# Optimization experiments

Hardware: AMD Instinct MI355X
Metric: run time of the kernel (lower is better)

The kernel has to match this reference:

```python
import jax, jax.numpy as jnp
import numpy as np

BATCH = 4
N1 = 131072   # stage-1 voxels (total over batch)
N2 = 32768    # stage-2 (stride-2 downsampled) voxels
D_MODEL = 128
D_INNER = 2 * D_MODEL
D_STATE = 16
D_CONV = 4
DT_RANK = 8   # ceil(d_model / 16)
EPS = 1e-5


def _ln(x, g, b):
    mu = x.mean(-1, keepdims=True)
    v = ((x - mu) ** 2).mean(-1, keepdims=True)
    return (x - mu) * jax.lax.rsqrt(v + EPS) * g + b


def _causal_conv(x, w, b):
    # x: [B,L,Di], w: [Di,K] -> depthwise causal conv1d
    y = jax.lax.conv_general_dilated(
        x.transpose(0, 2, 1), w[:, None, :], (1,), [(D_CONV - 1, 0)],
        dimension_numbers=('NCH', 'OIH', 'NCH'), feature_group_count=D_INNER)
    return y.transpose(0, 2, 1) + b


def _mamba_block(x, ln_g, ln_b, in_w, conv_w, conv_b, xproj_w, dtproj_w, dtproj_b, A_log, Dp, out_w):
    # create_block: LayerNorm -> Mamba mixer (selective scan); returns hidden states
    h = _ln(x, ln_g, ln_b)
    xz = h @ in_w.T                          # [B,L,2*Di]
    xc, z = jnp.split(xz, 2, axis=-1)
    xc = jax.nn.silu(_causal_conv(xc, conv_w, conv_b))
    dbl = xc @ xproj_w.T                     # [B,L,dt_rank+2*d_state]
    dt = jax.nn.softplus(dbl[..., :DT_RANK] @ dtproj_w.T + dtproj_b)  # [B,L,Di]
    Bm = dbl[..., DT_RANK:DT_RANK + D_STATE]
    Cm = dbl[..., DT_RANK + D_STATE:]
    A = -jnp.exp(A_log)                      # [Di,ds]

    def step(hst, inp):
        dt_t, b_t, c_t, u_t = inp            # [B,Di],[B,ds],[B,ds],[B,Di]
        hst = jnp.exp(dt_t[..., None] * A) * hst + (dt_t * u_t)[..., None] * b_t[:, None, :]
        return hst, jnp.einsum('bds,bs->bd', hst, c_t)

    h0 = jnp.zeros((x.shape[0], D_INNER, D_STATE), x.dtype)
    xs = (dt.transpose(1, 0, 2), Bm.transpose(1, 0, 2), Cm.transpose(1, 0, 2), xc.transpose(1, 0, 2))
    _, ys = jax.lax.scan(step, h0, xs)       # ys: [L,B,Di]
    y = ys.transpose(1, 0, 2) + xc * Dp
    y = y * jax.nn.silu(z)
    return y @ out_w.T


def _mamba_params(key):
    ks = jax.random.split(key, 6)
    s = lambda k, sh, sc: jax.random.normal(k, sh, jnp.float32) * sc
    return dict(
        ln_g=jnp.ones((D_MODEL,), jnp.float32), ln_b=jnp.zeros((D_MODEL,), jnp.float32),
        in_w=s(ks[0], (2 * D_INNER, D_MODEL), 0.05),
        conv_w=s(ks[1], (D_INNER, D_CONV), 0.2), conv_b=jnp.zeros((D_INNER,), jnp.float32),
        xproj_w=s(ks[2], (DT_RANK + 2 * D_STATE, D_INNER), 0.05),
        dtproj_w=s(ks[3], (D_INNER, DT_RANK), 0.1), dtproj_b=s(ks[4], (D_INNER,), 0.1),
        A_log=jnp.log(jnp.tile(jnp.arange(1, D_STATE + 1, dtype=jnp.float32), (D_INNER, 1))),
        D=jnp.ones((D_INNER,), jnp.float32),
        out_w=s(ks[5], (D_MODEL, D_INNER), 0.05))


def setup_inputs():
    key = jax.random.key(0)
    k = jax.random.split(key, 10)
    inp = {
        'feats_s1': jax.random.normal(k[0], (N1, D_MODEL), jnp.float32),
        'feats_s2': jax.random.normal(k[1], (N2, D_MODEL), jnp.float32),
        'pos_s1': jax.random.uniform(k[2], (N1, 3), jnp.float32),
        'pos_s2': jax.random.uniform(k[3], (N2, 3), jnp.float32),
        'hilbert_s1': jax.random.randint(k[4], (N1,), 0, 1 << 30, jnp.int32),
        'hilbert_s2': jax.random.randint(k[5], (N2,), 0, 1 << 30, jnp.int32),
        'pe_w': jax.random.normal(k[6], (D_MODEL, 3), jnp.float32) * 0.1,
        'pe_b': jnp.zeros((D_MODEL,), jnp.float32),
        'norm_g': jnp.ones((D_MODEL,), jnp.float32), 'norm_b': jnp.zeros((D_MODEL,), jnp.float32),
        'normb_g': jnp.ones((D_MODEL,), jnp.float32), 'normb_b': jnp.zeros((D_MODEL,), jnp.float32),
    }
    for pref, kk in (('m1_', k[7]), ('m2_', k[8])):
        for n, v in _mamba_params(kk).items():
            inp[pref + n] = v
    return inp


def _forward(feats_s1, feats_s2, pos_s1, pos_s2, pe_w, pe_b, norm_g, norm_b, normb_g, normb_b,
             m1_ln_g, m1_ln_b, m1_in_w, m1_conv_w, m1_conv_b, m1_xproj_w, m1_dtproj_w, m1_dtproj_b, m1_A_log, m1_D, m1_out_w,
             m2_ln_g, m2_ln_b, m2_in_w, m2_conv_w, m2_conv_b, m2_xproj_w, m2_dtproj_w, m2_dtproj_b, m2_A_log, m2_D, m2_out_w,
             hilbert_s1, hilbert_s2):
    L1, L2 = N1 // BATCH, N2 // BATCH
    m1 = (m1_ln_g, m1_ln_b, m1_in_w, m1_conv_w, m1_conv_b, m1_xproj_w, m1_dtproj_w, m1_dtproj_b, m1_A_log, m1_D, m1_out_w)
    m2 = (m2_ln_g, m2_ln_b, m2_in_w, m2_conv_w, m2_conv_b, m2_xproj_w, m2_dtproj_w, m2_dtproj_b, m2_A_log, m2_D, m2_out_w)

    # stage 2: hilbert-order forward scan through mamba_layer1
    f2 = (feats_s2 + pos_s2 @ pe_w.T + pe_b).reshape(BATCH, L2, D_MODEL)
    o2 = jnp.argsort(hilbert_s2.reshape(BATCH, L2), axis=-1)          # inds_curt_to_next
    seq2 = jnp.take_along_axis(f2, o2[..., None], axis=1)
    out2 = _mamba_block(seq2, *m1)
    back2 = jnp.take_along_axis(out2, jnp.argsort(o2, axis=-1)[..., None], axis=1).reshape(N2, D_MODEL)
    out_s2 = _ln(back2, norm_g, norm_b)

    # stage 1: flipped hilbert-order (backward) scan through mamba_layer2
    f1 = (feats_s1 + pos_s1 @ pe_w.T + pe_b).reshape(BATCH, L1, D_MODEL)
    o1 = jnp.argsort(hilbert_s1.reshape(BATCH, L1), axis=-1)
    seq1 = jnp.take_along_axis(f1, o1[..., None], axis=1)[:, ::-1, :]
    out1 = _mamba_block(seq1, *m2)[:, ::-1, :]
    back1 = jnp.take_along_axis(out1, jnp.argsort(o1, axis=-1)[..., None], axis=1).reshape(N1, D_MODEL)
    out_s1 = _ln(back1, normb_g, normb_b)

    return jnp.concatenate([out_s1, out_s2], axis=0)   # [N1+N2, d_model]


def reference(feats_s1, feats_s2, pos_s1, pos_s2, pe_w, pe_b, norm_g, norm_b, normb_g, normb_b,
              m1_ln_g, m1_ln_b, m1_in_w, m1_conv_w, m1_conv_b, m1_xproj_w, m1_dtproj_w, m1_dtproj_b, m1_A_log, m1_D, m1_out_w,
              m2_ln_g, m2_ln_b, m2_in_w, m2_conv_w, m2_conv_b, m2_xproj_w, m2_dtproj_w, m2_dtproj_b, m2_A_log, m2_D, m2_out_w,
              hilbert_s1, hilbert_s2):
    return _forward(feats_s1, feats_s2, pos_s1, pos_s2, pe_w, pe_b, norm_g, norm_b, normb_g, normb_b,
                    m1_ln_g, m1_ln_b, m1_in_w, m1_conv_w, m1_conv_b, m1_xproj_w, m1_dtproj_w, m1_dtproj_b, m1_A_log, m1_D, m1_out_w,
                    m2_ln_g, m2_ln_b, m2_in_w, m2_conv_w, m2_conv_b, m2_xproj_w, m2_dtproj_w, m2_dtproj_b, m2_A_log, m2_D, m2_out_w,
                    hilbert_s1, hilbert_s2)
```

## Files before the change

kernel.cpp:

```cpp
#include <hip/hip_runtime.h>
#include <hip/hip_bf16.h>

#define DEV __device__ __forceinline__

constexpr int BATCH_ = 4;
constexpr int N1_ = 131072;
constexpr int N2_ = 32768;
constexpr int L1_ = N1_ / BATCH_;
constexpr int L2_ = N2_ / BATCH_;
constexpr int DM_ = 128;
constexpr int DI_ = 256;
constexpr int DS_ = 16;
constexpr int DTR_ = 8;
constexpr int TOT_ = N1_ + N2_;

constexpr int TA_ = 32;
constexpr int TAH_ = TA_ + 3;
constexpr int NTILE1_ = L1_ / TA_;
constexpr int NTILE2_ = L2_ / TA_;
constexpr int NTILES_ = 4 * NTILE1_ + 4 * NTILE2_;

constexpr int TS_ = 64;
constexpr int NCH1_ = L1_ / TS_;
constexpr int NCH2_ = L2_ / TS_;
constexpr int NCHUNKS_ = 4 * NCH1_ + 4 * NCH2_;

constexpr int NST_ = 160;

constexpr int PADR_ = 16;
constexpr int SR1_ = L1_ + 2 * PADR_;
constexpr int SR2_ = L2_ + 2 * PADR_;
constexpr int RTOT_ = 4 * SR1_ + 4 * SR2_;

constexpr int IN1_OFF = 0;
constexpr int IN2_OFF = 65536;
constexpr int XP1_OFF = 131072;
constexpr int XP2_OFF = 143360;
constexpr int OW1_OFF = 155648;
constexpr int OW2_OFF = 188416;
constexpr int W16_TOT = 221184;

typedef short short8 __attribute__((ext_vector_type(8)));
typedef float f32x4 __attribute__((ext_vector_type(4)));

struct MP {
  const float* ln_g; const float* ln_b; const float* in_w;
  const float* conv_w; const float* conv_b; const float* xproj_w;
  const float* dtproj_w; const float* dtproj_b; const float* A_log;
  const float* Dp; const float* out_w;
};

DEV float softplusf(float x) {
  return fmaxf(x, 0.f) + __logf(1.f + __expf(-fabsf(x)));
}

DEV unsigned short f2bf(float f) {
  unsigned u = __builtin_bit_cast(unsigned, f);
  u += 0x7fffu + ((u >> 16) & 1u);
  return (unsigned short)(u >> 16);
}
DEV float bf2f(unsigned short s) {
  unsigned u = ((unsigned)s) << 16;
  return __builtin_bit_cast(float, u);
}

DEV void sort_tile_info(int tile, int& seg, int& tis, int& slotbase) {
  if (tile < 128) { seg = tile >> 5; tis = tile & 31; slotbase = seg * L1_; }
  else { seg = 4 + ((tile - 128) >> 3); tis = (tile - 128) & 7; slotbase = N1_ + (seg - 4) * L2_; }
}

__global__ __launch_bounds__(256) void k_prep(
    const float* __restrict__ in_w1, const float* __restrict__ xp1,
    const float* __restrict__ ow1,
    const float* __restrict__ in_w2, const float* __restrict__ xp2,
    const float* __restrict__ ow2,
    unsigned short* __restrict__ w16)
{
  const int i = blockIdx.x * 256 + threadIdx.x;
  if (i >= W16_TOT) return;
  float v;
  if (i < IN2_OFF) v = in_w1[i - IN1_OFF];
  else if (i < XP1_OFF) v = in_w2[i - IN2_OFF];
  else if (i < XP2_OFF) {
    const int j = i - XP1_OFF; const int r = j >> 8;
    v = (r < 40) ? xp1[j] : 0.f;
  } else if (i < OW1_OFF) {
    const int j = i - XP2_OFF; const int r = j >> 8;
    v = (r < 40) ? xp2[j] : 0.f;
  } else if (i < OW2_OFF) v = ow1[i - OW1_OFF];
  else v = ow2[i - OW2_OFF];
  w16[i] = f2bf(v);
}

__global__ __launch_bounds__(256) void k_hist(
    const int* __restrict__ hil1, const int* __restrict__ hil2,
    const unsigned* __restrict__ ksrc, unsigned* __restrict__ histg,
    int shift, int pass0)
{
  const int tile = blockIdx.x;
  int seg, tis, slotbase;
  sort_tile_info(tile, seg, tis, slotbase);
  const int tid = threadIdx.x;
  __shared__ unsigned h[1024];
  #pragma unroll
  for (int i = 0; i < 4; ++i) h[i * 256 + tid] = 0;
  __syncthreads();
  #pragma unroll
  for (int it = 0; it < 4; ++it) {
    const int li = tis * 1024 + it * 256 + tid;
    unsigned k;
    if (pass0) k = (unsigned)(seg < 4 ? hil1[seg * L1_ + li] : hil2[(seg - 4) * L2_ + li]);
    else       k = ksrc[slotbase + li];
    atomicAdd(&h[(k >> shift) & 1023u], 1u);
  }
  __syncthreads();
  #pragma unroll
  for (int i = 0; i < 4; ++i)
    histg[tile * 1024 + i * 256 + tid] = h[i * 256 + tid];
}

__global__ __launch_bounds__(256) void k_scanoff(
    const unsigned* __restrict__ histg, unsigned* __restrict__ offg)
{
  const int seg = blockIdx.x;
  const int ntiles = seg < 4 ? 32 : 8;
  const int tilebase = seg < 4 ? seg * 32 : 128 + (seg - 4) * 8;
  const int tid = threadIdx.x;
  const int d0 = tid * 4;
  unsigned tot[4] = {0, 0, 0, 0};
  for (int t = 0; t < ntiles; ++t) {
    const unsigned* hp = &histg[(size_t)(tilebase + t) * 1024 + d0];
    tot[0] += hp[0]; tot[1] += hp[1]; tot[2] += hp[2]; tot[3] += hp[3];
  }
  unsigned lp[4]; unsigned s = 0;
  #pragma unroll
  for (int j = 0; j < 4; ++j) { lp[j] = s; s += tot[j]; }
  const int lane = tid & 63, wv = tid >> 6;
  unsigned inc = s;
  #pragma unroll
  for (int off = 1; off < 64; off <<= 1) {
    unsigned v = (unsigned)__shfl_up((int)inc, off, 64);
    if (lane >= off) inc += v;
  }
  __shared__ unsigned wsum[4];
  if (lane == 63) wsum[wv] = inc;
  __syncthreads();
  unsigned wbase = 0;
  for (int w = 0; w < 4; ++w) if (w < wv) wbase += wsum[w];
  const unsigned base = wbase + inc - s;
  #pragma unroll
  for (int j = 0; j < 4; ++j) {
    unsigned run = base + lp[j];
    for (int t = 0; t < ntiles; ++t) {
      offg[(size_t)(tilebase + t) * 1024 + d0 + j] = run;
      run += histg[(size_t)(tilebase + t) * 1024 + d0 + j];
    }
  }
}

__global__ __launch_bounds__(256) void k_scatter(
    const int* __restrict__ hil1, const int* __restrict__ hil2,
    const unsigned* __restrict__ ksrc, const int* __restrict__ isrc,
    const unsigned* __restrict__ offg,
    unsigned* __restrict__ kdst, int* __restrict__ idst,
    int* __restrict__ o_all, int shift, int pass0, int last)
{
  const int tile = blockIdx.x;
  int seg, tis, slotbase;
  sort_tile_info(tile, seg, tis, slotbase);
  const int tid = threadIdx.x;
  const int lane = tid & 63, wv = tid >> 6;
  __shared__ unsigned runb[1024];
  __shared__ unsigned wcnt[4 * 1024];
  #pragma unroll
  for (int i = 0; i < 4; ++i) runb[i * 256 + tid] = offg[(size_t)tile * 1024 + i * 256 + tid];
  #pragma unroll
  for (int it = 0; it < 4; ++it) {
    #pragma unroll
    for (int i = 0; i < 16; ++i) wcnt[i * 256 + tid] = 0;
    __syncthreads();
    const int li = tis * 1024 + it * 256 + tid;
    unsigned k; int v;
    if (pass0) {
      k = (unsigned)(seg < 4 ? hil1[seg * L1_ + li] : hil2[(seg - 4) * L2_ + li]);
      v = li;
    } else {
      k = ksrc[slotbase + li]; v = isrc[slotbase + li];
    }
    const unsigned d = (k >> shift) & 1023u;
    unsigned long long m = ~0ull;
    #pragma unroll
    for (int b = 0; b < 10; ++b) {
      const unsigned long long bb = __ballot((int)((d >> b) & 1u));
      m &= ((d >> b) & 1u) ? bb : ~bb;
    }
    const unsigned lrank = (unsigned)__popcll(m & ((1ull << lane) - 1ull));
    wcnt[wv * 1024 + d] = (unsigned)__popcll(m);
    __syncthreads();
    unsigned prior = runb[d];
    for (int w = 0; w < 3; ++w) if (w < wv) prior += wcnt[w * 1024 + d];
    const unsigned pos = prior + lrank;
    if (last) o_all[slotbase + pos] = v;
    else { kdst[slotbase + pos] = k; idst[slotbase + pos] = v; }
    __syncthreads();
    #pragma unroll
    for (int i = 0; i < 4; ++i) {
      const int dd = i * 256 + tid;
      runb[dd] += wcnt[dd] + wcnt[1024 + dd] + wcnt[2048 + dd] + wcnt[3072 + dd];
    }
    __syncthreads();
  }
}

__global__ __launch_bounds__(256) void k_gather(
    const float* __restrict__ feats1, const float* __restrict__ feats2,
    const float* __restrict__ pos1, const float* __restrict__ pos2,
    const float* __restrict__ pe_w, const float* __restrict__ pe_b,
    MP p1, MP p2, const int* __restrict__ o_all,
    unsigned* __restrict__ seq_g)
{
  const int wv = threadIdx.x >> 6, lane = threadIdx.x & 63;
  const int prow = blockIdx.x * 4 + wv;
  if (prow >= RTOT_) return;
  int seg, within;
  if (prow < 4 * SR1_) { seg = prow / SR1_; within = prow - seg * SR1_; }
  else { const int r = prow - 4 * SR1_; seg = 4 + r / SR2_; within = r - (seg - 4) * SR2_; }
  const bool is1 = seg < 4;
  const int b = is1 ? seg : seg - 4;
  const int L = is1 ? L1_ : L2_;
  const int p = within - PADR_;
  unsigned outw = 0;
  if (p >= 0 && p < L) {
    const int slotbase = is1 ? b * L1_ : N1_ + b * L2_;
    const int orig = o_all[slotbase + p];
    const MP P = is1 ? p2 : p1;
    const float* fr = (is1 ? feats1 + (size_t)b * L1_ * DM_
                           : feats2 + (size_t)b * L2_ * DM_) + (size_t)orig * DM_;
    const float* pr = (is1 ? pos1 + (size_t)b * L1_ * 3
                           : pos2 + (size_t)b * L2_ * 3) + (size_t)orig * 3;
    const int c0 = 2 * lane;
    const float2 f = *(const float2*)(fr + c0);
    const float q0 = pr[0], q1 = pr[1], q2 = pr[2];
    float x0 = f.x + q0 * pe_w[c0 * 3 + 0] + q1 * pe_w[c0 * 3 + 1] + q2 * pe_w[c0 * 3 + 2] + pe_b[c0];
    float x1 = f.y + q0 * pe_w[c0 * 3 + 3] + q1 * pe_w[c0 * 3 + 4] + q2 * pe_w[c0 * 3 + 5] + pe_b[c0 + 1];
    float s = x0 + x1, qq = x0 * x0 + x1 * x1;
    #pragma unroll
    for (int off = 32; off; off >>= 1) {
      s += __shfl_xor(s, off, 64);
      qq += __shfl_xor(qq, off, 64);
    }
    const float mu = s * (1.f / 128.f);
    const float rs = rsqrtf(qq * (1.f / 128.f) - mu * mu + 1e-5f);
    const unsigned short o0 = f2bf((x0 - mu) * rs * P.ln_g[c0]     + P.ln_b[c0]);
    const unsigned short o1 = f2bf((x1 - mu) * rs * P.ln_g[c0 + 1] + P.ln_b[c0 + 1]);
    outw = (unsigned)o0 | ((unsigned)o1 << 16);
  }
  seq_g[(size_t)prow * 64 + lane] = outw;
}

constexpr int HB_ = 136;
constexpr int XB_ = 264;
constexpr int OFF_HB16 = TAH_ * XB_ * 2;
constexpr int SMEM_A = OFF_HB16 + 48 * HB_ * 2;

__global__ __launch_bounds__(256) void k_phaseA(
    MP p1, MP p2,
    const unsigned short* __restrict__ seq_g,
    const unsigned short* __restrict__ w16,
    __hip_bfloat16* __restrict__ xc_g, __hip_bfloat16* __restrict__ z_g,
    float* __restrict__ dbl_g)
{
  const int blk = blockIdx.x;
  bool is1; int b, tile;
  if (blk < 4 * NTILE1_) { is1 = true; b = blk / NTILE1_; tile = blk % NTILE1_; }
  else { const int r = blk - 4 * NTILE1_; is1 = false; b = r / NTILE2_; tile = r % NTILE2_; }
  const int slotbase = is1 ? b * L1_ : N1_ + b * L2_;
  const MP P = is1 ? p2 : p1;
  const unsigned short* iw16 = w16 + (is1 ? IN2_OFF : IN1_OFF);
  const unsigned short* xp16 = w16 + (is1 ? XP2_OFF : XP1_OFF);
  const int segrow0 = is1 ? b * SR1_ : 4 * SR1_ + b * SR2_;
  const unsigned short* seq = seq_g + (size_t)segrow0 * DM_;
  const bool rev = is1;
  const int t0 = tile * TA_;
  const int pstart = rev ? t0 : t0 - 3;
  const int lsh = rev ? 0 : 3;

  __shared__ char smem[SMEM_A];
  unsigned short* xcb16 = (unsigned short*)smem;
  unsigned short* hb16 = (unsigned short*)(smem + OFF_HB16);
  unsigned short* xc16 = xcb16;

  const int tid = threadIdx.x;
  const int lane = tid & 63, wv = tid >> 6;
  const int l15 = lane & 15, quad = lane >> 4;

  {
    unsigned* hz = (unsigned*)hb16;
    for (int i = tid; i < 13 * (HB_ / 2); i += 256)
      hz[TAH_ * (HB_ / 2) + i] = 0;
    const unsigned short* src = seq + (size_t)(PADR_ + pstart) * DM_;
    #pragma unroll
    for (int i = tid; i < TAH_ * 16; i += 256) {
      const int r = i >> 4, c = (i & 15) * 8;
      *(uint4*)(hb16 + r * HB_ + c) = *(const uint4*)(src + (size_t)r * DM_ + c);
    }
  }
  __syncthreads();
  {
    short8 afr[3][4];
    #pragma unroll
    for (int mt = 0; mt < 3; ++mt)
      #pragma unroll
      for (int t = 0; t < 4; ++t)
        afr[mt][t] = *(const short8*)(hb16 + (mt * 16 + l15) * HB_ + t * 32 + quad * 8);
    for (int nn = 0; nn < 8; ++nn) {
      const int ntile = nn * 4 + wv;
      f32x4 acc[3];
      #pragma unroll
      for (int mt = 0; mt < 3; ++mt) acc[mt] = (f32x4){0.f, 0.f, 0.f, 0.f};
      #pragma unroll
      for (int t = 0; t < 4; ++t) {
        const short8 bfr = *(const short8*)(iw16 + (size_t)(ntile * 16 + l15) * DM_ + t * 32 + quad * 8);
        #pragma unroll
        for (int mt = 0; mt < 3; ++mt)
          acc[mt] = __builtin_amdgcn_mfma_f32_16x16x32_bf16(afr[mt][t], bfr, acc[mt], 0, 0, 0);
      }
      const int col = ntile * 16 + l15;
      if (col < 256) {
        #pragma unroll
        for (int mt = 0; mt < 3; ++mt)
          #pragma unroll
          for (int r = 0; r < 4; ++r) {
            const int row = mt * 16 + quad * 4 + r;
            if (row < TAH_) xcb16[row * XB_ + col] = f2bf(acc[mt][r]);
          }
      } else {
        #pragma unroll
        for (int mt = 0; mt < 3; ++mt)
          #pragma unroll
          for (int r = 0; r < 4; ++r) {
            const int row = mt * 16 + quad * 4 + r;
            const int m = row - lsh;
            if (m >= 0 && m < TA_) {
              const float zz = acc[mt][r];
              const float sg = zz / (1.f + __expf(-zz));
              z_g[(size_t)(slotbase + t0 + m) * DI_ + (col - 256)] = __float2bfloat16(sg);
            }
          }
      }
    }
  }
  __syncthreads();
  {
    const int d = tid;
    const float w0 = P.conv_w[d * 4 + 0], w1 = P.conv_w[d * 4 + 1],
                w2 = P.conv_w[d * 4 + 2], w3 = P.conv_w[d * 4 + 3];
    const float cb = P.conv_b[d];
    float x0 = bf2f(xcb16[0 * XB_ + d]), x1 = bf2f(xcb16[1 * XB_ + d]),
          x2 = bf2f(xcb16[2 * XB_ + d]);
    #pragma unroll
    for (int m = 0; m < TA_; ++m) {
      const float x3 = bf2f(xcb16[(m + 3) * XB_ + d]);
      float v;
      if (rev) v = w3 * x0 + w2 * x1 + w1 * x2 + w0 * x3;
      else     v = w0 * x0 + w1 * x1 + w2 * x2 + w3 * x3;
      v += cb;
      v = v * (1.f / (1.f + __expf(-v)));
      const unsigned short vb = f2bf(v);
      xc_g[(size_t)(slotbase + t0 + m) * DI_ + d] = __builtin_bit_cast(__hip_bfloat16, vb);
      xcb16[m * XB_ + d] = vb;
      x0 = x1; x1 = x2; x2 = x3;
    }
  }
  __syncthreads();
  if (wv < 3) {
    f32x4 acc0 = (f32x4){0.f,0.f,0.f,0.f}, acc1 = acc0;
    #pragma unroll
    for (int t = 0; t < 8; ++t) {
      const short8 bfr = *(const short8*)(xp16 + (size_t)(wv * 16 + l15) * DI_ + t * 32 + quad * 8);
      const short8 a0 = *(const short8*)(xc16 + (l15) * XB_ + t * 32 + quad * 8);
      const short8 a1 = *(const short8*)(xc16 + (16 + l15) * XB_ + t * 32 + quad * 8);
      acc0 = __builtin_amdgcn_mfma_f32_16x16x32_bf16(a0, bfr, acc0, 0, 0, 0);
      acc1 = __builtin_amdgcn_mfma_f32_16x16x32_bf16(a1, bfr, acc1, 0, 0, 0);
    }
    const int col = wv * 16 + l15;
    if (col < 40) {
      #pragma unroll
      for (int r = 0; r < 4; ++r) {
        dbl_g[(size_t)(slotbase + t0 + quad * 4 + r) * 40 + col] = acc0[r];
        dbl_g[(size_t)(slotbase + t0 + 16 + quad * 4 + r) * 40 + col] = acc1[r];
      }
    }
  }
}

struct ScanP {
  float Av[DS_]; float A0; bool fast;
  float dtw[DTR_]; float dtb;
};
DEV void load_scanp(const MP& P, int d, ScanP& sp) {
  #pragma unroll
  for (int s = 0; s < DS_; ++s) sp.Av[s] = -__expf(P.A_log[d * DS_ + s]);
  sp.A0 = sp.Av[0];
  bool f = true;
  #pragma unroll
  for (int s = 0; s < DS_; ++s)
    f = f && (fabsf(sp.Av[s] - (float)(s + 1) * sp.A0) <= 1e-3f * (float)(s + 1));
  sp.fast = f;
  #pragma unroll
  for (int r = 0; r < DTR_; ++r) sp.dtw[r] = P.dtproj_w[d * DTR_ + r];
  sp.dtb = P.dtproj_b[d];
}
DEV float dt_from(const float4& q0, const float4& q1, const ScanP& sp) {
  const float dtraw = sp.dtb
      + q0.x*sp.dtw[0] + q0.y*sp.dtw[1] + q0.z*sp.dtw[2] + q0.w*sp.dtw[3]
      + q1.x*sp.dtw[4] + q1.y*sp.dtw[5] + q1.z*sp.dtw[6] + q1.w*sp.dtw[7];
  return softplusf(dtraw);
}

__global__ __launch_bounds__(256) void k_scan1(
    MP p1, MP p2,
    const __hip_bfloat16* __restrict__ xc_g, const float* __restrict__ dbl_g,
    float* __restrict__ hloc, float* __restrict__ sumdt_g)
{
  const int blk = blockIdx.x;
  bool is1; int b, pc;
  if (blk < 4 * NCH1_) { is1 = true; b = blk / NCH1_; pc = blk % NCH1_; }
  else { const int r = blk - 4 * NCH1_; is1 = false; b = r / NCH2_; pc = r % NCH2_; }
  const MP P = is1 ? p2 : p1;
  const int L = is1 ? L1_ : L2_;
  const bool rev = is1;
  const int slotbase = is1 ? b * L1_ : N1_ + b * L2_;
  const int d = threadIdx.x;
  ScanP sp; load_scanp(P, d, sp);
  const unsigned short* xcp = (const unsigned short*)xc_g;
  float h[DS_];
  #pragma unroll
  for (int s = 0; s < DS_; ++s) h[s] = 0.f;
  float sdt = 0.f;
  const int s0 = rev ? (L - (pc + 1) * TS_) : pc * TS_;
  const int dp = rev ? -1 : 1;
  int slot = slotbase + (rev ? (s0 + TS_ - 1) : s0);
  if (sp.fast) {
    #pragma unroll 2
    for (int i = 0; i < TS_; ++i) {
      const float* dr = dbl_g + (size_t)slot * 40;
      const float4 q0 = *(const float4*)dr, q1 = *(const float4*)(dr + 4);
      const float u = bf2f(xcp[(size_t)slot * DI_ + d]);
      float4 Bv[4];
      #pragma unroll
      for (int j = 0; j < 4; ++j) Bv[j] = *(const float4*)(dr + 8 + 4 * j);
      const float dt = dt_from(q0, q1, sp);
      const float du = dt * u;
      sdt += dt;
      const float e1 = __expf(dt * sp.A0);
      const float e2 = e1 * e1, e3 = e2 * e1, e4 = e2 * e2;
      float base = 1.f;
      #pragma unroll
      for (int j = 0; j < 4; ++j) {
        const float m1 = base * e1, m2 = base * e2, m3 = base * e3, m4 = base * e4;
        h[4*j+0] = m1 * h[4*j+0] + du * Bv[j].x;
        h[4*j+1] = m2 * h[4*j+1] + du * Bv[j].y;
        h[4*j+2] = m3 * h[4*j+2] + du * Bv[j].z;
        h[4*j+3] = m4 * h[4*j+3] + du * Bv[j].w;
        base = m4;
      }
      slot += dp;
    }
  } else {
    for (int i = 0; i < TS_; ++i) {
      const float* dr = dbl_g + (size_t)slot * 40;
      const float4 q0 = *(const float4*)dr, q1 = *(const float4*)(dr + 4);
      const float dt = dt_from(q0, q1, sp);
      const float u = bf2f(xcp[(size_t)slot * DI_ + d]);
      const float du = dt * u;
      sdt += dt;
      float Bvv[16];
      #pragma unroll
      for (int j = 0; j < 4; ++j) *(float4*)&Bvv[4*j] = *(const float4*)(dr + 8 + 4*j);
      #pragma unroll
      for (int s = 0; s < DS_; ++s)
        h[s] = __expf(dt * sp.Av[s]) * h[s] + du * Bvv[s];
      slot += dp;
    }
  }
  float* hl = hloc + (size_t)blk * DS_ * DI_;
  #pragma unroll
  for (int s = 0; s < DS_; ++s) hl[s * DI_ + d] = h[s];
  sumdt_g[(size_t)blk * DI_ + d] = sdt;
}

__global__ __launch_bounds__(256) void k_scan2(
    MP p1, MP p2, float* __restrict__ hloc,
    const float* __restrict__ sumdt_g)
{
  const int seq = blockIdx.x >> 4;
  const int s = blockIdx.x & 15;
  const bool is1 = seq < 4;
  const int b = is1 ? seq : seq - 4;
  const MP P = is1 ? p2 : p1;
  const int nch = is1 ? NCH1_ : NCH2_;
  const int chbase = is1 ? b * NCH1_ : 4 * NCH1_ + b * NCH2_;
  const int d = threadIdx.x;
  const float A = -__expf(P.A_log[d * DS_ + s]);
  float carry = 0.f;
  for (int pc = 0; pc < nch; ++pc) {
    const size_t idx = (size_t)(chbase + pc);
    const float sdt = sumdt_g[idx * DI_ + d];
    const float hl = hloc[idx * DS_ * DI_ + s * DI_ + d];
    hloc[idx * DS_ * DI_ + s * DI_ + d] = carry;
    carry = __expf(A * sdt) * carry + hl;
  }
}

__global__ __launch_bounds__(256) void k_scan3(
    MP p1, MP p2,
    const __hip_bfloat16* __restrict__ xc_g, const float* __restrict__ dbl_g,
    const float* __restrict__ hin, __hip_bfloat16* zv_g)
{
  const int blk = blockIdx.x;
  bool is1; int b, pc;
  if (blk < 4 * NCH1_) { is1 = true; b = blk / NCH1_; pc = blk % NCH1_; }
  else { const int r = blk - 4 * NCH1_; is1 = false; b = r / NCH2_; pc = r % NCH2_; }
  const MP P = is1 ? p2 : p1;
  const int L = is1 ? L1_ : L2_;
  const bool rev = is1;
  const int slotbase = is1 ? b * L1_ : N1_ + b * L2_;
  const int d = threadIdx.x;
  ScanP sp; load_scanp(P, d, sp);
  const float Dp = P.Dp[d];
  const unsigned short* xcp = (const unsigned short*)xc_g;
  unsigned short* zvp = (unsigned short*)zv_g;
  float h[DS_];
  const float* hi = hin + (size_t)blk * DS_ * DI_;
  #pragma unroll
  for (int s = 0; s < DS_; ++s) h[s] = hi[s * DI_ + d];
  const int s0 = rev ? (L - (pc + 1) * TS_) : pc * TS_;
  const int dp = rev ? -1 : 1;
  int slot = slotbase + (rev ? (s0 + TS_ - 1) : s0);
  if (sp.fast) {
    float sz = bf2f(zvp[(size_t)slot * DI_ + d]);
    #pragma unroll 2
    for (int i = 0; i < TS_; ++i) {
      const int nslot = (i + 1 < TS_) ? slot + dp : slot;
      const float nsz = bf2f(zvp[(size_t)nslot * DI_ + d]);
      const float* dr = dbl_g + (size_t)slot * 40;
      const float4 q0 = *(const float4*)dr, q1 = *(const float4*)(dr + 4);
      const float u = bf2f(xcp[(size_t)slot * DI_ + d]);
      float4 Bv[4], Cv[4];
      #pragma unroll
      for (int j = 0; j < 4; ++j) {
        Bv[j] = *(const float4*)(dr + 8 + 4 * j);
        Cv[j] = *(const float4*)(dr + 24 + 4 * j);
      }
      const float dt = dt_from(q0, q1, sp);
      const float du = dt * u;
      const float e1 = __expf(dt * sp.A0);
      const float e2 = e1 * e1, e3 = e2 * e1, e4 = e2 * e2;
      float base = 1.f, y = 0.f;
      #pragma unroll
      for (int j = 0; j < 4; ++j) {
        const float m1 = base * e1, m2 = base * e2, m3 = base * e3, m4 = base * e4;
        h[4*j+0] = m1 * h[4*j+0] + du * Bv[j].x;  y += h[4*j+0] * Cv[j].x;
        h[4*j+1] = m2 * h[4*j+1] + du * Bv[j].y;  y += h[4*j+1] * Cv[j].y;
        h[4*j+2] = m3 * h[4*j+2] + du * Bv[j].z;  y += h[4*j+2] * Cv[j].z;
        h[4*j+3] = m4 * h[4*j+3] + du * Bv[j].w;  y += h[4*j+3] * Cv[j].w;
        base = m4;
      }
      zvp[(size_t)slot * DI_ + d] = f2bf((y + u * Dp) * sz);
      slot = nslot; sz = nsz;
    }
  } else {
    for (int i = 0; i < TS_; ++i) {
      const float* dr = dbl_g + (size_t)slot * 40;
      const float4 q0 = *(const float4*)dr, q1 = *(const float4*)(dr + 4);
      const float dt = dt_from(q0, q1, sp);
      const float u = bf2f(xcp[(size_t)slot * DI_ + d]);
      const float sz = bf2f(zvp[(size_t)slot * DI_ + d]);
      const float du = dt * u;
      float Bvv[16], Cvv[16];
      #pragma unroll
      for (int j = 0; j < 4; ++j) {
        *(float4*)&Bvv[4*j] = *(const float4*)(dr + 8 + 4*j);
        *(float4*)&Cvv[4*j] = *(const float4*)(dr + 24 + 4*j);
      }
      float y = 0.f;
      #pragma unroll
      for (int s = 0; s < DS_; ++s) {
        h[s] = __expf(dt * sp.Av[s]) * h[s] + du * Bvv[s];
        y += h[s] * Cvv[s];
      }
      zvp[(size_t)slot * DI_ + d] = f2bf((y + u * Dp) * sz);
      slot += dp;
    }
  }
}

constexpr int OB_ = 132;
__global__ __launch_bounds__(256) void k_final(
    const __hip_bfloat16* __restrict__ v_g, const int* __restrict__ o_all,
    const unsigned short* __restrict__ w16,
    const float* __restrict__ norm_g, const float* __restrict__ norm_b,
    const float* __restrict__ normb_g, const float* __restrict__ normb_b,
    float* __restrict__ out)
{
  const int blk = blockIdx.x;
  bool is1; int b, tile;
  if (blk < 4 * NTILE1_) { is1 = true; b = blk / NTILE1_; tile = blk % NTILE1_; }
  else { const int r = blk - 4 * NTILE1_; is1 = false; b = r / NTILE2_; tile = r % NTILE2_; }
  const unsigned short* W = w16 + (is1 ? OW2_OFF : OW1_OFF);
  const float* gg = is1 ? normb_g : norm_g;
  const float* gb = is1 ? normb_b : norm_b;
  const int slotbase = is1 ? b * L1_ : N1_ + b * L2_;
  const int t0 = tile * TA_;
  __shared__ float obuf[TA_ * OB_];
  const int tid = threadIdx.x;
  const int lane = tid & 63, wv = tid >> 6;
  const int l15 = lane & 15, quad = lane >> 4;
  {
    const unsigned short* vp = (const unsigned short*)v_g + (size_t)(slotbase + t0) * DI_;
    f32x4 acc00 = (f32x4){0.f,0.f,0.f,0.f}, acc01 = acc00, acc10 = acc00, acc11 = acc00;
    #pragma unroll
    for (int t = 0; t < 8; ++t) {
      const short8 a0 = *(const short8*)(vp + (size_t)(l15) * DI_ + t * 32 + quad * 8);
      const short8 a1 = *(const short8*)(vp + (size_t)(16 + l15) * DI_ + t * 32 + quad * 8);
      const short8 b0 = *(const short8*)(W + (size_t)((wv) * 16 + l15) * DI_ + t * 32 + quad * 8);
      const short8 b1 = *(const short8*)(W + (size_t)((wv + 4) * 16 + l15) * DI_ + t * 32 + quad * 8);
      acc00 = __builtin_amdgcn_mfma_f32_16x16x32_bf16(a0, b0, acc00, 0, 0, 0);
      acc01 = __builtin_amdgcn_mfma_f32_16x16x32_bf16(a1, b0, acc01, 0, 0, 0);
      acc10 = __builtin_amdgcn_mfma_f32_16x16x32_bf16(a0, b1, acc10, 0, 0, 0);
      acc11 = __builtin_amdgcn_mfma_f32_16x16x32_bf16(a1, b1, acc11, 0, 0, 0);
    }
    const int col0 = wv * 16 + l15;
    const int col1 = (wv + 4) * 16 + l15;
    #pragma unroll
    for (int r = 0; r < 4; ++r) {
      obuf[(quad * 4 + r) * OB_ + col0] = acc00[r];
      obuf[(16 + quad * 4 + r) * OB_ + col0] = acc01[r];
      obuf[(quad * 4 + r) * OB_ + col1] = acc10[r];
      obuf[(16 + quad * 4 + r) * OB_ + col1] = acc11[r];
    }
  }
  __syncthreads();
  {
    for (int m = wv; m < TA_; m += 4) {
      float x0 = obuf[m * OB_ + lane], x1 = obuf[m * OB_ + lane + 64];
      float s = x0 + x1, q = x0 * x0 + x1 * x1;
      #pragma unroll
      for (int off = 32; off; off >>= 1) {
        s += __shfl_xor(s, off, 64);
        q += __shfl_xor(q, off, 64);
      }
      const float mu = s * (1.f / 128.f);
      const float rs = rsqrtf(q * (1.f / 128.f) - mu * mu + 1e-5f);
      const int orig = o_all[slotbase + t0 + m];
      float* orow = out + (size_t)(slotbase + orig) * DM_;
      orow[lane]      = (x0 - mu) * rs * gg[lane]      + gb[lane];
      orow[lane + 64] = (x1 - mu) * rs * gg[lane + 64] + gb[lane + 64];
    }
  }
}

extern "C" void kernel_launch(void* const* d_in, const int* in_sizes, int n_in,
                              void* d_out, int out_size, void* d_ws, size_t ws_size,
                              hipStream_t stream)
{
  (void)in_sizes; (void)n_in; (void)out_size; (void)ws_size;
  const float* feats1 = (const float*)d_in[0];
  const float* feats2 = (const float*)d_in[1];
  const float* pos1   = (const float*)d_in[2];
  const float* pos2   = (const float*)d_in[3];
  const int*   hil1   = (const int*)d_in[4];
  const int*   hil2   = (const int*)d_in[5];
  const float* pe_w   = (const float*)d_in[6];
  const float* pe_b   = (const float*)d_in[7];
  const float* norm_g  = (const float*)d_in[8];
  const float* norm_b  = (const float*)d_in[9];
  const float* normb_g = (const float*)d_in[10];
  const float* normb_b = (const float*)d_in[11];
  MP p1 { (const float*)d_in[12], (const float*)d_in[13], (const float*)d_in[14],
          (const float*)d_in[15], (const float*)d_in[16], (const float*)d_in[17],
          (const float*)d_in[18], (const float*)d_in[19], (const float*)d_in[20],
          (const float*)d_in[21], (const float*)d_in[22] };
  MP p2 { (const float*)d_in[23], (const float*)d_in[24], (const float*)d_in[25],
          (const float*)d_in[26], (const float*)d_in[27], (const float*)d_in[28],
          (const float*)d_in[29], (const float*)d_in[30], (const float*)d_in[31],
          (const float*)d_in[32], (const float*)d_in[33] };

  char* w = (char*)d_ws;
  auto take = [&](size_t bytes) -> char* {
    char* p = w; w += (bytes + 255) & ~(size_t)255; return p;
  };
  int* o_all = (int*)take((size_t)TOT_ * 4);
  char* uni = take((size_t)RTOT_ * DM_ * 2);
  unsigned* kA = (unsigned*)(uni);
  int*      iA = (int*)     (uni + (size_t)TOT_ * 4);
  unsigned* kB = (unsigned*)(uni + (size_t)TOT_ * 8);
  int*      iB = (int*)     (uni + (size_t)TOT_ * 12);
  unsigned* histg = (unsigned*)(uni + (size_t)TOT_ * 16);
  unsigned* offg  = (unsigned*)(uni + (size_t)TOT_ * 16 + (size_t)NST_ * 1024 * 4);
  unsigned* seq = (unsigned*)uni;
  __hip_bfloat16* xc = (__hip_bfloat16*)take((size_t)TOT_ * DI_ * 2);
  __hip_bfloat16* vzb = (__hip_bfloat16*)take((size_t)TOT_ * DI_ * 2);
  float* dbl = (float*)take((size_t)TOT_ * 40 * 4);
  float* hloc = (float*)take((size_t)NCHUNKS_ * DS_ * DI_ * 4);
  float* sdt  = (float*)take((size_t)NCHUNKS_ * DI_ * 4);
  unsigned short* w16 = (unsigned short*)take((size_t)W16_TOT * 2);

  hipLaunchKernelGGL(k_prep, dim3((W16_TOT + 255) / 256), dim3(256), 0, stream,
                     p1.in_w, p1.xproj_w, p1.out_w, p2.in_w, p2.xproj_w, p2.out_w, w16);
  hipLaunchKernelGGL(k_hist, dim3(NST_), dim3(256), 0, stream,
                     hil1, hil2, kB, histg, 0, 1);
  hipLaunchKernelGGL(k_scanoff, dim3(8), dim3(256), 0, stream, histg, offg);
  hipLaunchKernelGGL(k_scatter, dim3(NST_), dim3(256), 0, stream,
                     hil1, hil2, kB, iB, offg, kB, iB, o_all, 0, 1, 0);
  hipLaunchKernelGGL(k_hist, dim3(NST_), dim3(256), 0, stream,
                     hil1, hil2, kB, histg, 10, 0);
  hipLaunchKernelGGL(k_scanoff, dim3(8), dim3(256), 0, stream, histg, offg);
  hipLaunchKernelGGL(k_scatter, dim3(NST_), dim3(256), 0, stream,
                     hil1, hil2, kB, iB, offg, kA, iA, o_all, 10, 0, 0);
  hipLaunchKernelGGL(k_hist, dim3(NST_), dim3(256), 0, stream,
                     hil1, hil2, kA, histg, 20, 0);
  hipLaunchKernelGGL(k_scanoff, dim3(8), dim3(256), 0, stream, histg, offg);
  hipLaunchKernelGGL(k_scatter, dim3(NST_), dim3(256), 0, stream,
                     hil1, hil2, kA, iA, offg, kB, iB, o_all, 20, 0, 1);

  hipLaunchKernelGGL(k_gather, dim3((RTOT_ + 3) / 4), dim3(256), 0, stream,
                     feats1, feats2, pos1, pos2, pe_w, pe_b, p1, p2, o_all, seq);
  hipLaunchKernelGGL(k_phaseA, dim3(NTILES_), dim3(256), 0, stream,
                     p1, p2, (const unsigned short*)seq, w16, xc, vzb, dbl);
  hipLaunchKernelGGL(k_scan1, dim3(NCHUNKS_), dim3(256), 0, stream,
                     p1, p2, xc, dbl, hloc, sdt);
  hipLaunchKernelGGL(k_scan2, dim3(128), dim3(256), 0, stream,
                     p1, p2, hloc, sdt);
  hipLaunchKernelGGL(k_scan3, dim3(NCHUNKS_), dim3(256), 0, stream,
                     p1, p2, xc, dbl, hloc, vzb);
  hipLaunchKernelGGL(k_final, dim3(NTILES_), dim3(256), 0, stream,
                     vzb, o_all, w16, norm_g, norm_b, normb_g, normb_b,
                     (float*)d_out);
}
```

Baseline: 913.8 us.

## Split inter-chunk scan carry into two-level hierarchical scan over chunk groups

Replaces the single serial pass over all chunks per sequence with a two-level scan. Groups of 32 chunks are scanned in parallel first, a short serial scan then runs over group totals, and the group carry is folded into each chunk's initial state in the final scan kernel using prefix sums of dt. The aim is to remove the long serial dependency chain in the old 128-block carry kernel, which ran up to 512 sequential steps with very low occupancy. The cost is an extra kernel launch, extra buffers reused from the sort scratch area, and some extra exp work when computing initial states.

New measurement: 799.6 us. 1.14x faster.

```diff
diff --git a/kernel.cpp b/kernel.cpp
--- a/kernel.cpp
+++ b/kernel.cpp
@@ -25,6 +25,11 @@
 constexpr int NCH2_ = L2_ / TS_;
 constexpr int NCHUNKS_ = 4 * NCH1_ + 4 * NCH2_;
 
+constexpr int GRP_ = 32;
+constexpr int NG1_ = NCH1_ / GRP_;
+constexpr int NG2_ = NCH2_ / GRP_;
+constexpr int NGRPS_ = 4 * NG1_ + 4 * NG2_;
+
 constexpr int NST_ = 160;
 
 constexpr int PADR_ = 16;
@@ -67,6 +72,11 @@
 DEV void sort_tile_info(int tile, int& seg, int& tis, int& slotbase) {
   if (tile < 128) { seg = tile >> 5; tis = tile & 31; slotbase = seg * L1_; }
   else { seg = 4 + ((tile - 128) >> 3); tis = (tile - 128) & 7; slotbase = N1_ + (seg - 4) * L2_; }
+}
+
+DEV void group_info(int g, bool& is1, int& chbase) {
+  if (g < 4 * NG1_) { is1 = true; chbase = (g >> 4) * NCH1_ + (g & 15) * GRP_; }
+  else { const int r = g - 4 * NG1_; is1 = false; chbase = 4 * NCH1_ + (r >> 2) * NCH2_ + (r & 3) * GRP_; }
 }
 
 __global__ __launch_bounds__(256) void k_prep(
@@ -490,33 +500,61 @@
   sumdt_g[(size_t)blk * DI_ + d] = sdt;
 }
 
-__global__ __launch_bounds__(256) void k_scan2(
+__global__ __launch_bounds__(256) void k_scan2a(
     MP p1, MP p2, float* __restrict__ hloc,
-    const float* __restrict__ sumdt_g)
+    const float* __restrict__ sumdt_g,
+    float* __restrict__ Sg, float* __restrict__ presum_g,
+    float* __restrict__ gsum_g)
+{
+  const int g = blockIdx.x >> 4;
+  const int s = blockIdx.x & 15;
+  bool is1; int chbase;
+  group_info(g, is1, chbase);
+  const MP P = is1 ? p2 : p1;
+  const int d = threadIdx.x;
+  const float A = -__expf(P.A_log[d * DS_ + s]);
+  float carry = 0.f, run = 0.f;
+  for (int pc = 0; pc < GRP_; ++pc) {
+    const size_t idx = (size_t)(chbase + pc);
+    const float sdt = sumdt_g[idx * DI_ + d];
+    const float hl = hloc[idx * DS_ * DI_ + s * DI_ + d];
+    hloc[idx * DS_ * DI_ + s * DI_ + d] = carry;
+    carry = __expf(A * sdt) * carry + hl;
+    if (s == 0) presum_g[idx * DI_ + d] = run;
+    run += sdt;
+  }
+  Sg[((size_t)g * DS_ + s) * DI_ + d] = carry;
+  if (s == 0) gsum_g[(size_t)g * DI_ + d] = run;
+}
+
+__global__ __launch_bounds__(256) void k_scan2b(
+    MP p1, MP p2, float* __restrict__ Sg,
+    const float* __restrict__ gsum_g)
 {
   const int seq = blockIdx.x >> 4;
   const int s = blockIdx.x & 15;
   const bool is1 = seq < 4;
   const int b = is1 ? seq : seq - 4;
   const MP P = is1 ? p2 : p1;
-  const int nch = is1 ? NCH1_ : NCH2_;
-  const int chbase = is1 ? b * NCH1_ : 4 * NCH1_ + b * NCH2_;
+  const int ng = is1 ? NG1_ : NG2_;
+  const int gbase = is1 ? b * NG1_ : 4 * NG1_ + b * NG2_;
   const int d = threadIdx.x;
   const float A = -__expf(P.A_log[d * DS_ + s]);
-  float carry = 0.f;
-  for (int pc = 0; pc < nch; ++pc) {
-    const size_t idx = (size_t)(chbase + pc);
-    const float sdt = sumdt_g[idx * DI_ + d];
-    const float hl = hloc[idx * DS_ * DI_ + s * DI_ + d];
-    hloc[idx * DS_ * DI_ + s * DI_ + d] = carry;
-    carry = __expf(A * sdt) * carry + hl;
+  float C = 0.f;
+  for (int gi = 0; gi < ng; ++gi) {
+    const int g = gbase + gi;
+    const float gs = gsum_g[(size_t)g * DI_ + d];
+    const float sgv = Sg[((size_t)g * DS_ + s) * DI_ + d];
+    Sg[((size_t)g * DS_ + s) * DI_ + d] = C;
+    C = __expf(A * gs) * C + sgv;
   }
 }
 
 __global__ __launch_bounds__(256) void k_scan3(
     MP p1, MP p2,
     const __hip_bfloat16* __restrict__ xc_g, const float* __restrict__ dbl_g,
-    const float* __restrict__ hin, __hip_bfloat16* zv_g)
+    const float* __restrict__ hin, const float* __restrict__ Cg_g,
+    const float* __restrict__ presum_g, __hip_bfloat16* zv_g)
 {
   const int blk = blockIdx.x;
   bool is1; int b, pc;
@@ -531,10 +569,21 @@
   const float Dp = P.Dp[d];
   const unsigned short* xcp = (const unsigned short*)xc_g;
   unsigned short* zvp = (unsigned short*)zv_g;
+  const int g = (blk < 4 * NCH1_) ? (blk / GRP_) : (4 * NG1_ + (blk - 4 * NCH1_) / GRP_);
+  const float ps = presum_g[(size_t)blk * DI_ + d];
+  const float* cg = Cg_g + ((size_t)g * DS_) * DI_ + d;
   float h[DS_];
   const float* hi = hin + (size_t)blk * DS_ * DI_;
-  #pragma unroll
-  for (int s = 0; s < DS_; ++s) h[s] = hi[s * DI_ + d];
+  if (sp.fast) {
+    const float e1p = __expf(sp.A0 * ps);
+    float m = e1p;
+    #pragma unroll
+    for (int s = 0; s < DS_; ++s) { h[s] = hi[s * DI_ + d] + cg[s * DI_] * m; m *= e1p; }
+  } else {
+    #pragma unroll
+    for (int s = 0; s < DS_; ++s)
+      h[s] = hi[s * DI_ + d] + cg[s * DI_] * __expf(sp.Av[s] * ps);
+  }
   const int s0 = rev ? (L - (pc + 1) * TS_) : pc * TS_;
   const int dp = rev ? -1 : 1;
   int slot = slotbase + (rev ? (s0 + TS_ - 1) : s0);
@@ -700,6 +749,10 @@
   unsigned* histg = (unsigned*)(uni + (size_t)TOT_ * 16);
   unsigned* offg  = (unsigned*)(uni + (size_t)TOT_ * 16 + (size_t)NST_ * 1024 * 4);
   unsigned* seq = (unsigned*)uni;
+  float* Sg     = (float*)uni;
+  float* presum = (float*)(uni + (size_t)NGRPS_ * DS_ * DI_ * 4);
+  float* gsum   = (float*)(uni + (size_t)NGRPS_ * DS_ * DI_ * 4
+                               + (size_t)NCHUNKS_ * DI_ * 4);
   __hip_bfloat16* xc = (__hip_bfloat16*)take((size_t)TOT_ * DI_ * 2);
   __hip_bfloat16* vzb = (__hip_bfloat16*)take((size_t)TOT_ * DI_ * 2);
   float* dbl = (float*)take((size_t)TOT_ * 40 * 4);
@@ -731,10 +784,12 @@
                      p1, p2, (const unsigned short*)seq, w16, xc, vzb, dbl);
   hipLaunchKernelGGL(k_scan1, dim3(NCHUNKS_), dim3(256), 0, stream,
                      p1, p2, xc, dbl, hloc, sdt);
-  hipLaunchKernelGGL(k_scan2, dim3(128), dim3(256), 0, stream,
-                     p1, p2, hloc, sdt);
+  hipLaunchKernelGGL(k_scan2a, dim3(NGRPS_ * DS_), dim3(256), 0, stream,
+                     p1, p2, hloc, sdt, Sg, presum, gsum);
+  hipLaunchKernelGGL(k_scan2b, dim3(128), dim3(256), 0, stream,
+                     p1, p2, Sg, gsum);
   hipLaunchKernelGGL(k_scan3, dim3(NCHUNKS_), dim3(256), 0, stream,
-                     p1, p2, xc, dbl, hloc, vzb);
+                     p1, p2, xc, dbl, hloc, Sg, presum, vzb);
   hipLaunchKernelGGL(k_final, dim3(NTILES_), dim3(256), 0, stream,
                      vzb, o_all, w16, norm_g, norm_b, normb_g, normb_b,
                      (float*)d_out);
```
